# Kernel optimization log

Measured on AMD Instinct MI355X. Metric: run time of the kernel, lower is better.

## Reference

```python
import jax, jax.numpy as jnp
import numpy as np

N, T, D, H, E, ED = 4096, 16, 5, 128, 32768, 32

def _leaky(x):
    return jnp.where(x >= 0, x, 0.2 * x)

def _lstm(x, Wih, Whh, bih, bhh):
    # x: [N, T, D] -> hidden sequence [N, T, H]; PyTorch gate order i,f,g,o
    pre = jnp.einsum('ntd,gd->tng', x, Wih) + bih + bhh  # [T, N, 4H]
    Hd = Whh.shape[1]
    def step(carry, p):
        h, c = carry
        g = p + h @ Whh.T
        i, f, gg, o = jnp.split(g, 4, axis=-1)
        c = jax.nn.sigmoid(f) * c + jax.nn.sigmoid(i) * jnp.tanh(gg)
        h = jax.nn.sigmoid(o) * jnp.tanh(c)
        return (h, c), h
    z = jnp.zeros((x.shape[0], Hd), x.dtype)
    _, hs = jax.lax.scan(step, (z, z), pre)
    return jnp.swapaxes(hs, 0, 1)

def _sire(x, src, dst, efeat, Wq, bq, Wk, bk, We, be, Wr, br):
    # SIREConv with agg_type='sum': m = LeakyReLU(eq[dst]+ek[src]+e); sum over in-edges; then linear_relation
    eq = x @ Wq.T + bq            # [N, T, H]
    ek = x @ Wk.T + bk            # [N, T, H]
    e = efeat @ We.T + be         # [E, H]
    m = _leaky(eq[dst] + ek[src] + e[:, None, :])  # [E, T, H]
    ft = jax.ops.segment_sum(m, dst, num_segments=x.shape[0])  # [N, T, H]
    return ft @ Wr.T + br

def _forward(stock_features, srcs, dsts, efeats, sire_ps, lstm_p, attn_p, mlp_p):
    sf = stock_features / jnp.mean(stock_features, axis=1, keepdims=True)
    sr = _lstm(sf, *lstm_p)  # [N, T, H]
    outs = [sr]
    for s, d, ef, p in zip(srcs, dsts, efeats, sire_ps):
        outs.append(_sire(sr, s, d, ef, *p))
    cat = jnp.concatenate(outs, axis=-1)  # [N, T, 4H]
    aw = jax.nn.softmax(cat @ attn_p[0].T + attn_p[1], axis=-2)  # softmax over time
    pooled = jnp.sum(cat * aw, axis=-2)   # [N, 4H]
    W1, b1, W2, b2 = mlp_p
    h = _leaky(pooled @ W1.T + b1)
    out = _leaky(h @ W2.T + b2)           # [N, 1]
    return out / sf[:, -1, 0:1] - 1.0


def setup_inputs() -> dict:
    key = jax.random.key(0)
    ks = iter(jax.random.split(key, 64))
    def nrm(shape, s=0.05):
        return jax.random.normal(next(ks), shape, jnp.float32) * s
    inp = {}
    inp['stock_features'] = jax.random.uniform(next(ks), (N, T, D), jnp.float32) + 0.5
    for g in ['wiki', 'industry', 'corr']:
        inp[g + '_src'] = jax.random.randint(next(ks), (E,), 0, N, jnp.int32)
        inp[g + '_dst'] = jax.random.randint(next(ks), (E,), 0, N, jnp.int32)
        inp[g + '_efeat'] = nrm((E, ED), 1.0)
        inp[g + '_Wq'] = nrm((H, H)); inp[g + '_bq'] = nrm((H,))
        inp[g + '_Wk'] = nrm((H, H)); inp[g + '_bk'] = nrm((H,))
        inp[g + '_We'] = nrm((H, ED)); inp[g + '_be'] = nrm((H,))
        inp[g + '_Wr'] = nrm((H, H)); inp[g + '_br'] = nrm((H,))
    inp['lstm_Wih'] = nrm((4 * H, D)); inp['lstm_Whh'] = nrm((4 * H, H))
    inp['lstm_bih'] = nrm((4 * H,)); inp['lstm_bhh'] = nrm((4 * H,))
    inp['attn_W'] = nrm((1, 4 * H)); inp['attn_b'] = nrm((1,))
    inp['mlp_W1'] = nrm((H, 4 * H)); inp['mlp_b1'] = nrm((H,))
    inp['mlp_W2'] = nrm((1, H)); inp['mlp_b2'] = nrm((1,))
    return inp


def reference(stock_features, wiki_src, wiki_dst, wiki_efeat,
              wiki_Wq, wiki_bq, wiki_Wk, wiki_bk, wiki_We, wiki_be, wiki_Wr, wiki_br,
              industry_src, industry_dst, industry_efeat,
              industry_Wq, industry_bq, industry_Wk, industry_bk, industry_We, industry_be, industry_Wr, industry_br,
              corr_src, corr_dst, corr_efeat,
              corr_Wq, corr_bq, corr_Wk, corr_bk, corr_We, corr_be, corr_Wr, corr_br,
              lstm_Wih, lstm_Whh, lstm_bih, lstm_bhh,
              attn_W, attn_b, mlp_W1, mlp_b1, mlp_W2, mlp_b2):
    srcs = (wiki_src, industry_src, corr_src)
    dsts = (wiki_dst, industry_dst, corr_dst)
    efeats = (wiki_efeat, industry_efeat, corr_efeat)
    sire_ps = ((wiki_Wq, wiki_bq, wiki_Wk, wiki_bk, wiki_We, wiki_be, wiki_Wr, wiki_br),
               (industry_Wq, industry_bq, industry_Wk, industry_bk, industry_We, industry_be, industry_Wr, industry_br),
               (corr_Wq, corr_bq, corr_Wk, corr_bk, corr_We, corr_be, corr_Wr, corr_br))
    return _forward(stock_features, srcs, dsts, efeats, sire_ps,
                    (lstm_Wih, lstm_Whh, lstm_bih, lstm_bhh),
                    (attn_W, attn_b), (mlp_W1, mlp_b1, mlp_W2, mlp_b2))
```

## Files before the change

### kernel.cpp

```cpp
#include <hip/hip_runtime.h>
#include <cstdint>
#include <cstddef>

#define NS 4096
#define TS 16
#define DF 5
#define HD 128
#define EE 32768
#define EDD 32

typedef _Float16 h16;
typedef __attribute__((ext_vector_type(8))) _Float16 f16x8;
typedef __attribute__((ext_vector_type(2))) __fp16 fp16x2_n;
typedef __attribute__((ext_vector_type(4))) float f32x4;

__device__ __forceinline__ float sigmoidf_(float x){ return 1.f/(1.f+__expf(-x)); }
__device__ __forceinline__ float tanhf_(float x){ return 1.f - 2.f/(1.f+__expf(2.f*x)); }
__device__ __forceinline__ float leaky_(float x){ return x >= 0.f ? x : 0.2f*x; }

__device__ __forceinline__ unsigned pkh(float a, float b){
  union { fp16x2_n h; unsigned u; } x;
  x.h = __builtin_amdgcn_cvt_pkrtz(a, b);
  return x.u;
}
__device__ __forceinline__ void unpkh(unsigned u, float& a, float& b){
  union { unsigned u; fp16x2_n h; } x; x.u = u;
  a = (float)x.h.x; b = (float)x.h.y;
}
__device__ __forceinline__ f16x8 ld_h8(const h16* p){
  union { uint4 u; f16x8 v; } x; x.u = *(const uint4*)p; return x.v;
}

template<int AH, int CH>
__device__ __forceinline__ void gemm_dev(const void* Av, int lda,
    const float* __restrict__ Bp, int ldb, const float* __restrict__ bp,
    void* Cv, int ldc, int K, int act, size_t m0,
    h16* Asb, h16* Bsb)
{
  int tid = threadIdx.x;
  int wv = tid>>6, lane = tid&63, lm = lane&15, lq = lane>>4;
  f32x4 acc[2][8];
  #pragma unroll
  for (int mt=0;mt<2;mt++)
    #pragma unroll
    for (int nt=0;nt<8;nt++)
      acc[mt][nt] = (f32x4){0.f,0.f,0.f,0.f};

  for (int k0=0; k0<K; k0+=32){
    if (AH){
      const h16* A = (const h16*)Av;
      #pragma unroll
      for (int rep=0;rep<2;rep++){
        int idx = tid + rep*256;
        int row = idx>>2, c8 = idx&3;
        *(uint4*)&Asb[row*40 + c8*8] = *(const uint4*)&A[(m0+row)*(size_t)lda + k0 + c8*8];
      }
    } else {
      const float* A = (const float*)Av;
      #pragma unroll
      for (int rep=0;rep<4;rep++){
        int idx = tid + rep*256;
        int row = idx>>3, c4 = idx&7;
        float4 a = *(const float4*)&A[(m0+row)*(size_t)lda + k0 + c4*4];
        *(uint2*)&Asb[row*40 + c4*4] = make_uint2(pkh(a.x,a.y), pkh(a.z,a.w));
      }
    }
    #pragma unroll
    for (int rep=0;rep<4;rep++){
      int idx = tid + rep*256;
      int row = idx>>3, c4 = idx&7;
      float4 b = *(const float4*)&Bp[(size_t)row*ldb + k0 + c4*4];
      *(uint2*)&Bsb[row*40 + c4*4] = make_uint2(pkh(b.x,b.y), pkh(b.z,b.w));
    }
    __syncthreads();
    f16x8 afr[2], bfr[8];
    #pragma unroll
    for (int mt=0;mt<2;mt++)
      afr[mt] = ld_h8(&Asb[(wv*32 + mt*16 + lm)*40 + lq*8]);
    #pragma unroll
    for (int nt=0;nt<8;nt++)
      bfr[nt] = ld_h8(&Bsb[(nt*16 + lm)*40 + lq*8]);
    #pragma unroll
    for (int mt=0;mt<2;mt++)
      #pragma unroll
      for (int nt=0;nt<8;nt++)
        acc[mt][nt] = __builtin_amdgcn_mfma_f32_16x16x32_f16(afr[mt], bfr[nt], acc[mt][nt], 0,0,0);
    __syncthreads();
  }

  #pragma unroll
  for (int mt=0;mt<2;mt++){
    #pragma unroll
    for (int nt=0;nt<8;nt++){
      int col = nt*16 + lm;
      float bv = bp[col];
      #pragma unroll
      for (int i=0;i<4;i++){
        float o = acc[mt][nt][i] + bv;
        if (act) o = leaky_(o);
        size_t ridx = (m0 + wv*32 + mt*16 + lq*4 + i)*(size_t)ldc + col;
        if (CH) ((h16*)Cv)[ridx] = (h16)o;
        else    ((float*)Cv)[ridx] = o;
      }
    }
  }
}

__device__ void lstm8_dev(int blk, const float* __restrict__ sf,
                          const h16* __restrict__ WhhH,
                          const float* __restrict__ Wih, const float* __restrict__ bih,
                          const float* __restrict__ bhh, h16* __restrict__ cat,
                          char* smem)
{
  float* gates = (float*)smem;
  h16* hbuf = (h16*)(smem+16512);
  float* sfb = (float*)(smem+16512+2176);
  int tid = threadIdx.x;
  int n0 = blk*8;
  int wv = tid>>6, lane = tid&63, lm = lane&15, lq = lane>>4;

  f16x8 bfr[8][4];
  #pragma unroll
  for (int nt=0;nt<8;nt++){
    int g = wv*128 + nt*16 + lm;
    #pragma unroll
    for (int kt=0;kt<4;kt++)
      bfr[nt][kt] = *(const f16x8*)&WhhH[g*128 + kt*32 + lq*8];
  }

  int j = tid & 127;
  int rb = tid >> 7;
  float wih[4][5]; float bsum[4];
  #pragma unroll
  for (int gi=0; gi<4; gi++){
    int gc = gi*128 + j;
    #pragma unroll
    for (int d=0; d<5; d++) wih[gi][d] = Wih[gc*5+d];
    bsum[gi] = bih[gc] + bhh[gc];
  }
  float cst[4] = {0.f,0.f,0.f,0.f};

  for (int i=tid;i<544;i+=256) ((unsigned*)hbuf)[i] = 0;
  for (int i=tid;i<640;i+=256) sfb[i] = sf[(size_t)n0*80 + i];
  __syncthreads();

  f16x8 zf = {0,0,0,0,0,0,0,0};
  for (int t=0;t<16;t++){
    f16x8 af[4];
    #pragma unroll
    for (int kt=0;kt<4;kt++)
      af[kt] = (lm < 8) ? *(const f16x8*)&hbuf[lm*136 + kt*32 + lq*8] : zf;
    #pragma unroll
    for (int nt=0;nt<8;nt++){
      f32x4 acc = {0.f,0.f,0.f,0.f};
      #pragma unroll
      for (int kt=0;kt<4;kt++)
        acc = __builtin_amdgcn_mfma_f32_16x16x32_f16(af[kt], bfr[nt][kt], acc, 0,0,0);
      if (lq < 2){
        int col = wv*128 + nt*16 + lm;
        #pragma unroll
        for (int i=0;i<4;i++)
          gates[(lq*4+i)*516 + col] = acc[i];
      }
    }
    __syncthreads();
    #pragma unroll
    for (int q=0;q<4;q++){
      int r = rb + 2*q;
      const float* s = &sfb[r*80 + t*5];
      float pre[4];
      #pragma unroll
      for (int gi=0;gi<4;gi++){
        float a = bsum[gi];
        #pragma unroll
        for (int d=0;d<5;d++) a = fmaf(s[d], wih[gi][d], a);
        pre[gi] = a + gates[r*516 + gi*128 + j];
      }
      float iv = sigmoidf_(pre[0]);
      float fv = sigmoidf_(pre[1]);
      float gv = tanhf_(pre[2]);
      float ov = sigmoidf_(pre[3]);
      float c = fv*cst[q] + iv*gv;
      cst[q] = c;
      float h = ov*tanhf_(c);
      h16 hh = (h16)h;
      hbuf[r*136 + j] = hh;
      cat[(size_t)((n0+r)*16 + t)*512 + j] = hh;
    }
    __syncthreads();
  }
}

__global__ __launch_bounds__(256)
void k_prolog(const float* __restrict__ x, float* __restrict__ sf,
              const float* __restrict__ Whh, h16* __restrict__ whhH,
              int* __restrict__ cnt)
{
  int b = blockIdx.x, tid = threadIdx.x;
  if (b < 48){
    int i = b*256 + tid;
    if (i < 3*4096) cnt[i] = 0;
  } else if (b < 128){
    int id = (b-48)*256 + tid;
    if (id < NS*DF){
      int n = id / DF, d = id % DF;
      const float* xp = x + (size_t)n*TS*DF + d;
      float s = 0.f;
      #pragma unroll
      for (int t=0;t<TS;t++) s += xp[t*DF];
      float inv = (float)TS / s;
      float* sp = sf + (size_t)n*TS*DF + d;
      #pragma unroll
      for (int t=0;t<TS;t++) sp[t*DF] = xp[t*DF]*inv;
    }
  } else {
    int i = (b-128)*256 + tid;
    whhH[i] = (h16)Whh[i];
  }
}

struct M1 {
  const float *sf, *Wih, *bih, *bhh;
  const h16* WhhH;
  h16* cat;
  const float *ef[3]; const float *We[3]; const float *be[3];
  h16* eeb;
  const int* dst[3]; const int* src[3];
  int* cnt;
  int2* eidx2;
};
__global__ __launch_bounds__(256,2)
void k_mega1(M1 p)
{
  __shared__ __align__(16) char smem[21504];
  int b = blockIdx.x;
  if (b < 512){
    lstm8_dev(b, p.sf, p.WhhH, p.Wih, p.bih, p.bhh, p.cat, smem);
  } else if (b < 1280){
    int idx = b - 512;
    int proj = idx % 3, mt = idx / 3;
    h16* Asb = (h16*)smem;
    h16* Bsb = Asb + 128*40;
    gemm_dev<0,1>(p.ef[proj], 32, p.We[proj], 32, p.be[proj],
                  p.eeb + (size_t)proj*EE*128, 128, 32, 0, (size_t)mt*128, Asb, Bsb);
  } else {
    int idx = b - 1280;
    int g = idx >> 7, blk = idx & 127;
    int e = blk*256 + threadIdx.x;
    int d = p.dst[g][e];
    int s = p.src[g][e];
    int pos = atomicAdd(&p.cnt[g*4096 + d], 1);
    if (pos < 32) p.eidx2[((size_t)(g*4096 + d))*32 + pos] = make_int2(e, s);
  }
}

struct M2 {
  const h16* cat;
  const float* W[6]; const float* bias[6];
  h16* eqk;
};
__global__ __launch_bounds__(256)
void k_mega2(M2 p)
{
  __shared__ __align__(16) h16 Asb[128*40];
  __shared__ __align__(16) h16 Bsb[128*40];
  int b = blockIdx.x;
  int proj = b % 6, mt = b / 6;
  gemm_dev<1,1>(p.cat, 512, p.W[proj], 128, p.bias[proj],
                p.eqk + (size_t)proj*NS*TS*128, 128, 128, 0, (size_t)mt*128, Asb, Bsb);
}

__global__ __launch_bounds__(256)
void k_edge(const h16* __restrict__ eqk, const h16* __restrict__ eeb,
            const int* __restrict__ cnt, const int2* __restrict__ eidx2,
            h16* __restrict__ ft_)
{
  int n = blockIdx.x;
  int g = blockIdx.y;
  const h16* eqb = eqk + (size_t)(2*g)  *NS*TS*128;
  const h16* ekb = eqk + (size_t)(2*g+1)*NS*TS*128;
  const h16* eeg = eeb + (size_t)g*EE*128;
  h16* ft = ft_ + (size_t)g*NS*TS*128;
  int tid = threadIdx.x;
  int t = tid>>4, hb = (tid&15)*8;
  size_t own = ((size_t)(n*16+t))*128 + hb;
  f16x8 eqv = ld_h8(&eqb[own]);
  const f16x8 c02 = {(h16)0.2f,(h16)0.2f,(h16)0.2f,(h16)0.2f,
                     (h16)0.2f,(h16)0.2f,(h16)0.2f,(h16)0.2f};
  float acc[8];
  #pragma unroll
  for (int j=0;j<8;j++) acc[j]=0.f;
  int ne = cnt[g*4096 + n]; if (ne > 32) ne = 32;
  const int2* el = eidx2 + ((size_t)(g*4096 + n))*32;
  for (int i=0;i<ne;i++){
    int2 es = el[i];
    f16x8 kv = ld_h8(&ekb[((size_t)(es.y*16+t))*128 + hb]);
    f16x8 ev = ld_h8(&eeg[(size_t)es.x*128 + hb]);
    f16x8 x = eqv + kv + ev;
    f16x8 lk = __builtin_elementwise_max(x, x*c02);
    #pragma unroll
    for (int j=0;j<8;j++) acc[j] += (float)lk[j];
  }
  uint4 o;
  o.x = pkh(acc[0],acc[1]); o.y = pkh(acc[2],acc[3]);
  o.z = pkh(acc[4],acc[5]); o.w = pkh(acc[6],acc[7]);
  *(uint4*)&ft[own] = o;
}

struct WrP {
  const h16* A[3];
  const float* B[3]; const float* bias[3];
  h16* C[3];
};
__global__ __launch_bounds__(256)
void k_wr(WrP p)
{
  __shared__ __align__(16) h16 Asb[128*40];
  __shared__ __align__(16) h16 Bsb[128*40];
  int proj = blockIdx.x;
  size_t m0 = (size_t)blockIdx.y * 128;
  gemm_dev<1,1>(p.A[proj], 128, p.B[proj], 128, p.bias[proj],
                p.C[proj], 512, 128, 0, m0, Asb, Bsb);
}

__global__ __launch_bounds__(256)
void k_attn(const h16* __restrict__ cat, const float* __restrict__ attnW,
            const float* __restrict__ attnB, h16* __restrict__ pooled)
{
  __shared__ h16 ct[16*512];
  __shared__ float sred[4][16];
  int n = blockIdx.x, tid = threadIdx.x;
  {
    const uint4* srcp = (const uint4*)(cat + (size_t)n*8192);
    uint4* dstp = (uint4*)ct;
    for (int i=tid;i<1024;i+=256) dstp[i] = srcp[i];
  }
  __syncthreads();
  int c0 = tid*2;
  float w0 = attnW[c0], w1 = attnW[c0+1];
  const unsigned* ctu = (const unsigned*)ct;
  float loc[16];
  #pragma unroll
  for (int t=0;t<16;t++){
    float a,b; unpkh(ctu[t*256 + tid], a, b);
    loc[t] = a*w0 + b*w1;
  }
  #pragma unroll
  for (int t=0;t<16;t++){
    float v = loc[t];
    for (int off=1; off<64; off<<=1) v += __shfl_xor(v, off, 64);
    loc[t]=v;
  }
  int wave = tid >> 6, lane = tid & 63;
  if (lane==0){
    #pragma unroll
    for (int t=0;t<16;t++) sred[wave][t]=loc[t];
  }
  __syncthreads();
  float s[16]; float m=-1e30f;
  float ab = attnB[0];
  #pragma unroll
  for (int t=0;t<16;t++){ s[t] = sred[0][t]+sred[1][t]+sred[2][t]+sred[3][t] + ab; m = fmaxf(m, s[t]); }
  float sum=0.f;
  #pragma unroll
  for (int t=0;t<16;t++){ s[t] = __expf(s[t]-m); sum += s[t]; }
  float inv = 1.f/sum;
  float p0=0.f,p1=0.f;
  #pragma unroll
  for (int t=0;t<16;t++){
    float a = s[t]*inv;
    float x,y; unpkh(ctu[t*256 + tid], x, y);
    p0 = fmaf(x, a, p0); p1 = fmaf(y, a, p1);
  }
  ((unsigned*)pooled)[(size_t)n*256 + tid] = pkh(p0,p1);
}

__global__ __launch_bounds__(256)
void k_mlp(const h16* __restrict__ pooled, const float* __restrict__ W1,
           const float* __restrict__ b1, h16* __restrict__ hmlp,
           const float* __restrict__ W2, const float* __restrict__ b2,
           const float* __restrict__ sf, float* __restrict__ out)
{
  __shared__ __align__(16) h16 Asb[128*40];
  __shared__ __align__(16) h16 Bsb[128*40];
  size_t m0 = (size_t)blockIdx.x*128;
  gemm_dev<1,1>(pooled, 512, W1, 512, b1, hmlp, 128, 512, 1, m0, Asb, Bsb);
  __syncthreads();
  int tid = threadIdx.x;
  int r = tid >> 1, o64 = (tid & 1)*64;
  const h16* hp = hmlp + (m0 + r)*128 + o64;
  float acc = 0.f;
  #pragma unroll
  for (int c=0; c<64; c++) acc = fmaf((float)hp[c], W2[o64 + c], acc);
  acc += __shfl_xor(acc, 1, 64);
  if ((tid & 1) == 0){
    float o = leaky_(acc + b2[0]);
    size_t n = m0 + r;
    out[n] = o / sf[n*80 + 75] - 1.f;
  }
}

extern "C" void kernel_launch(void* const* d_in, const int* in_sizes, int n_in,
                              void* d_out, int out_size, void* d_ws, size_t ws_size,
                              hipStream_t stream)
{
  const float* x    = (const float*)d_in[0];
  const float* Wih  = (const float*)d_in[34];
  const float* Whh  = (const float*)d_in[35];
  const float* bih  = (const float*)d_in[36];
  const float* bhh  = (const float*)d_in[37];
  const float* attnW= (const float*)d_in[38];
  const float* attnB= (const float*)d_in[39];
  const float* W1   = (const float*)d_in[40];
  const float* b1   = (const float*)d_in[41];
  const float* W2   = (const float*)d_in[42];
  const float* b2   = (const float*)d_in[43];

  char* w = (char*)d_ws;
  size_t o = 0;
  h16* cat    = (h16*)(w+o); o += (size_t)NS*TS*512*2;
  h16* eqk    = (h16*)(w+o); o += (size_t)6*NS*TS*128*2;
  h16* eeb    = (h16*)(w+o); o += (size_t)3*EE*128*2;
  h16* ft     = (h16*)(w+o); o += (size_t)3*NS*TS*128*2;
  h16* pooled = (h16*)(w+o); o += (size_t)NS*512*2;
  float* sf   = (float*)(w+o); o += (size_t)NS*TS*DF*4;
  h16* hmlp   = (h16*)(w+o); o += (size_t)NS*HD*2;
  h16* whhH   = (h16*)(w+o); o += (size_t)512*128*2;
  int* cnt    = (int*)(w+o); o += 3*4096*4;
  int2* eidx2 = (int2*)(w+o); o += (size_t)3*4096*32*8;

  k_prolog<<<384, 256, 0, stream>>>(x, sf, Whh, whhH, cnt);

  {
    M1 p;
    p.sf = sf; p.Wih = Wih; p.bih = bih; p.bhh = bhh;
    p.WhhH = whhH; p.cat = cat; p.eeb = eeb; p.cnt = cnt; p.eidx2 = eidx2;
    for (int g=0; g<3; g++){
      int base = 1 + g*11;
      p.src[g] = (const int*)d_in[base+0];
      p.dst[g] = (const int*)d_in[base+1];
      p.ef[g] = (const float*)d_in[base+2];
      p.We[g] = (const float*)d_in[base+7];
      p.be[g] = (const float*)d_in[base+8];
    }
    k_mega1<<<1664, 256, 0, stream>>>(p);
  }

  {
    M2 p;
    p.cat = cat; p.eqk = eqk;
    for (int g=0; g<3; g++){
      int base = 1 + g*11;
      p.W[2*g]      = (const float*)d_in[base+3];
      p.bias[2*g]   = (const float*)d_in[base+4];
      p.W[2*g+1]    = (const float*)d_in[base+5];
      p.bias[2*g+1] = (const float*)d_in[base+6];
    }
    k_mega2<<<3072, 256, 0, stream>>>(p);
  }

  k_edge<<<dim3(NS,3), 256, 0, stream>>>(eqk, eeb, cnt, eidx2, ft);

  {
    WrP p;
    for (int g=0; g<3; g++){
      int base = 1 + g*11;
      p.A[g]    = ft + (size_t)g*NS*TS*128;
      p.B[g]    = (const float*)d_in[base+9];
      p.bias[g] = (const float*)d_in[base+10];
      p.C[g]    = cat + (size_t)(1+g)*128;
    }
    k_wr<<<dim3(3,512), 256, 0, stream>>>(p);
  }

  k_attn<<<NS, 256, 0, stream>>>(cat, attnW, attnB, pooled);
  k_mlp<<<32, 256, 0, stream>>>(pooled, W1, b1, hmlp, W2, b2, sf, (float*)d_out);
}
```

Baseline: 374.6 us.

## Fuse edge aggregation with Wr projection using per-block MFMA

Merges the edge sum kernel and the Wr linear GEMM into one kernel. Each block aggregates its node's 16x128 feature tile into shared memory, then multiplies it by Wr using MFMA and writes directly into cat. This removes the ft intermediate buffer and one launch, but every block reloads and converts the full 128x128 Wr matrix and uses more LDS.

```diff
diff --git a/kernel.cpp b/kernel.cpp
--- a/kernel.cpp
+++ b/kernel.cpp
@@ -270,18 +270,30 @@
                 p.eqk + (size_t)proj*NS*TS*128, 128, 128, 0, (size_t)mt*128, Asb, Bsb);
 }
 
+struct EWP { const float* Wr[3]; const float* br[3]; };
 __global__ __launch_bounds__(256)
-void k_edge(const h16* __restrict__ eqk, const h16* __restrict__ eeb,
-            const int* __restrict__ cnt, const int2* __restrict__ eidx2,
-            h16* __restrict__ ft_)
-{
+void k_edgewr(const h16* __restrict__ eqk, const h16* __restrict__ eeb,
+              const int* __restrict__ cnt, const int2* __restrict__ eidx2,
+              EWP wp, h16* __restrict__ cat)
+{
+  __shared__ __align__(16) h16 WrS[128*136];
+  __shared__ __align__(16) h16 ftS[16*136];
   int n = blockIdx.x;
   int g = blockIdx.y;
   const h16* eqb = eqk + (size_t)(2*g)  *NS*TS*128;
   const h16* ekb = eqk + (size_t)(2*g+1)*NS*TS*128;
   const h16* eeg = eeb + (size_t)g*EE*128;
-  h16* ft = ft_ + (size_t)g*NS*TS*128;
   int tid = threadIdx.x;
+
+  const float* Wr = wp.Wr[g];
+  #pragma unroll
+  for (int it=0; it<16; it++){
+    int r4 = tid + it*256;
+    int row = r4 >> 5, c4 = r4 & 31;
+    float4 v = *(const float4*)&Wr[row*128 + c4*4];
+    *(uint2*)&WrS[row*136 + c4*4] = make_uint2(pkh(v.x,v.y), pkh(v.z,v.w));
+  }
+
   int t = tid>>4, hb = (tid&15)*8;
   size_t own = ((size_t)(n*16+t))*128 + hb;
   f16x8 eqv = ld_h8(&eqb[own]);
@@ -304,23 +316,33 @@
   uint4 o;
   o.x = pkh(acc[0],acc[1]); o.y = pkh(acc[2],acc[3]);
   o.z = pkh(acc[4],acc[5]); o.w = pkh(acc[6],acc[7]);
-  *(uint4*)&ft[own] = o;
-}
-
-struct WrP {
-  const h16* A[3];
-  const float* B[3]; const float* bias[3];
-  h16* C[3];
-};
-__global__ __launch_bounds__(256)
-void k_wr(WrP p)
-{
-  __shared__ __align__(16) h16 Asb[128*40];
-  __shared__ __align__(16) h16 Bsb[128*40];
-  int proj = blockIdx.x;
-  size_t m0 = (size_t)blockIdx.y * 128;
-  gemm_dev<1,1>(p.A[proj], 128, p.B[proj], 128, p.bias[proj],
-                p.C[proj], 512, 128, 0, m0, Asb, Bsb);
+  *(uint4*)&ftS[t*136 + hb] = o;
+  __syncthreads();
+
+  int wv = tid>>6, lane = tid&63, lm = lane&15, lq = lane>>4;
+  f16x8 af[4];
+  #pragma unroll
+  for (int kt=0;kt<4;kt++)
+    af[kt] = ld_h8(&ftS[lm*136 + kt*32 + lq*8]);
+  const float* br = wp.br[g];
+  h16* catp = cat + (size_t)(1+g)*128;
+  #pragma unroll
+  for (int nn=0; nn<2; nn++){
+    int nt = wv*2 + nn;
+    f32x4 a2 = {0.f,0.f,0.f,0.f};
+    #pragma unroll
+    for (int kt=0;kt<4;kt++){
+      f16x8 bf = ld_h8(&WrS[(nt*16+lm)*136 + kt*32 + lq*8]);
+      a2 = __builtin_amdgcn_mfma_f32_16x16x32_f16(af[kt], bf, a2, 0,0,0);
+    }
+    int colg = nt*16 + lm;
+    float bv = br[colg];
+    #pragma unroll
+    for (int i=0;i<4;i++){
+      int row = lq*4 + i;
+      catp[((size_t)(n*16+row))*512 + colg] = (h16)(a2[i] + bv);
+    }
+  }
 }
 
 __global__ __launch_bounds__(256)
@@ -421,7 +443,6 @@
   h16* cat    = (h16*)(w+o); o += (size_t)NS*TS*512*2;
   h16* eqk    = (h16*)(w+o); o += (size_t)6*NS*TS*128*2;
   h16* eeb    = (h16*)(w+o); o += (size_t)3*EE*128*2;
-  h16* ft     = (h16*)(w+o); o += (size_t)3*NS*TS*128*2;
   h16* pooled = (h16*)(w+o); o += (size_t)NS*512*2;
   float* sf   = (float*)(w+o); o += (size_t)NS*TS*DF*4;
   h16* hmlp   = (h16*)(w+o); o += (size_t)NS*HD*2;
@@ -459,18 +480,14 @@
     k_mega2<<<3072, 256, 0, stream>>>(p);
   }
 
-  k_edge<<<dim3(NS,3), 256, 0, stream>>>(eqk, eeb, cnt, eidx2, ft);
-
   {
-    WrP p;
+    EWP wp;
     for (int g=0; g<3; g++){
       int base = 1 + g*11;
-      p.A[g]    = ft + (size_t)g*NS*TS*128;
-      p.B[g]    = (const float*)d_in[base+9];
-      p.bias[g] = (const float*)d_in[base+10];
-      p.C[g]    = cat + (size_t)(1+g)*128;
-    }
-    k_wr<<<dim3(3,512), 256, 0, stream>>>(p);
+      wp.Wr[g] = (const float*)d_in[base+9];
+      wp.br[g] = (const float*)d_in[base+10];
+    }
+    k_edgewr<<<dim3(NS,3), 256, 0, stream>>>(eqk, eeb, cnt, eidx2, wp, cat);
   }
 
   k_attn<<<NS, 256, 0, stream>>>(cat, attnW, attnB, pooled);
```

New measurement: 370.9 us. No clear change (-1.0%).
